# Kernel tuning notes

Measured on AMD Instinct MI355X. Metric: run time of the kernel, lower is better.

The kernel has to match this reference:

```python
import jax, jax.numpy as jnp
import numpy as np
import math

B, T, D_IN, D_F, H = 256, 64, 2048, 2048, 512


def _uniform(key, shape, stdv):
    return jax.random.uniform(key, shape, jnp.float32, -stdv, stdv)


def setup_inputs() -> dict:
    key = jax.random.key(0)
    ks = jax.random.split(key, 16)
    stdv = 1.0 / math.sqrt(H)
    return {
        "input_feats": jax.random.normal(ks[0], (B, T, D_IN), jnp.float32),
        "aux0": jax.random.normal(ks[1], (B, T, D_F), jnp.float32),
        "W_ih": _uniform(ks[2], (3 * H, D_IN), stdv),
        "b_ih": _uniform(ks[3], (3 * H,), stdv),
        "W_fh0": _uniform(ks[4], (2 * H, D_F), stdv),
        "b_fh0": _uniform(ks[5], (2 * H,), stdv),
        "W_hh": _uniform(ks[6], (3 * H, H), stdv),
        "b_hh": _uniform(ks[7], (3 * H,), stdv),
        "Wq": _uniform(ks[8], (H, H), stdv),
        "bq": _uniform(ks[9], (H,), stdv),
        "Wk": _uniform(ks[10], (H, H), stdv),
        "bk": _uniform(ks[11], (H,), stdv),
        "Wv": _uniform(ks[12], (H, H), stdv),
        "bv": _uniform(ks[13], (H,), stdv),
    }


def _gru_gcc_forward(input_feats, aux0, W_ih, b_ih, W_fh0, b_fh0, W_hh, b_hh,
                     Wq, bq, Wk, bk, Wv, bv):
    # Precompute input and aux projections for all timesteps (big batched GEMMs).
    gi_all = jnp.einsum('btd,gd->btg', input_feats, W_ih) + b_ih   # [B,T,3H]
    gf_all = jnp.einsum('btd,gd->btg', aux0, W_fh0) + b_fh0        # [B,T,2H]
    scale = 1.0 / math.sqrt(H)

    def attend(q, kv_in):
        # q: [B,1,H], kv_in: [B,S,H] raw gate candidates (keys == values)
        k = jnp.einsum('bsh,oh->bso', kv_in, Wk) + bk
        v = jnp.einsum('bsh,oh->bso', kv_in, Wv) + bv
        scores = jnp.einsum('bqh,bsh->bqs', q, k) * scale
        p = jax.nn.softmax(scores, axis=-1)
        return jnp.einsum('bqs,bsh->bqh', p, v)[:, 0, :]  # [B,H]

    def step(hx, xs):
        gi_t, gf_t = xs  # [B,3H], [B,2H]
        gh = hx @ W_hh.T + b_hh
        i_r, i_i, i_n = jnp.split(gi_t, 3, axis=1)
        h_r, h_i, h_n = jnp.split(gh, 3, axis=1)
        t1, t2 = jnp.split(gf_t, 2, axis=1)
        q = jnp.einsum('bqh,oh->bqo', hx[:, None, :], Wq) + bq  # [B,1,H]
        keys_r = jnp.stack([t1, i_r], axis=1)  # [B,2,H]
        keys_i = jnp.stack([t2, i_i], axis=1)
        resetgate = jax.nn.sigmoid(attend(q, keys_r) + h_r)
        inputgate = jax.nn.sigmoid(attend(q, keys_i) + h_i)
        newgate = jnp.tanh(i_n + resetgate * h_n)
        hy = newgate + inputgate * (hx - newgate)
        return hy, hy

    hx0 = jnp.zeros((input_feats.shape[0], H), input_feats.dtype)
    xs = (jnp.swapaxes(gi_all, 0, 1), jnp.swapaxes(gf_all, 0, 1))  # time-major
    h_last, out = jax.lax.scan(step, hx0, xs)
    return jnp.swapaxes(out, 0, 1), h_last  # [B,T,H], [B,H]


def reference(input_feats, aux0, W_ih, b_ih, W_fh0, b_fh0, W_hh, b_hh,
              Wq, bq, Wk, bk, Wv, bv):
    return _gru_gcc_forward(input_feats, aux0, W_ih, b_ih, W_fh0, b_fh0,
                            W_hh, b_hh, Wq, bq, Wk, bk, Wv, bv)
```

## Files before the change

kernel.cpp:

```cpp
#include <hip/hip_runtime.h>
#include <hip/hip_bf16.h>
#include <cstdint>
#include <cstddef>

#define B_    256
#define T_    64
#define H_    512
#define DIN_  2048
#define BT_   (B_ * T_)
#define NPRE_ 2560
#define NCAT_ 2048
#define NV_   2048

typedef __attribute__((ext_vector_type(8))) __bf16 bf16x8;
typedef __attribute__((ext_vector_type(4))) float  f32x4;

__device__ __forceinline__ float bf2f(unsigned short u) {
    union { unsigned int i; float f; } v; v.i = ((unsigned int)u) << 16; return v.f;
}
__device__ __forceinline__ unsigned short f2bf(float f) {
    union { float f; unsigned int i; } v; v.f = f;
    unsigned int x = v.i;
    return (unsigned short)((x + 0x7fffu + ((x >> 16) & 1u)) >> 16);
}

__device__ __forceinline__ void gload_lds16(const unsigned short* g, unsigned short* l) {
    __builtin_amdgcn_global_load_lds(
        (const __attribute__((address_space(1))) void*)g,
        (__attribute__((address_space(3))) void*)l, 16, 0, 0);
}

__global__ void cast4_kernel(const float* __restrict__ src,
                             unsigned short* __restrict__ dst, int n4) {
    int i = blockIdx.x * blockDim.x + threadIdx.x;
    if (i >= n4) return;
    const float4 v = ((const float4*)src)[i];
    ushort4 o;
    o.x = f2bf(v.x); o.y = f2bf(v.y); o.z = f2bf(v.z); o.w = f2bf(v.w);
    ((ushort4*)dst)[i] = o;
}

__global__ __launch_bounds__(256)
void wqk_kernel(const float* __restrict__ Wk, const float* __restrict__ Wq,
                unsigned short* __restrict__ Wout) {
    __shared__ float sk[16][17], sq[16][17];
    const int tid = threadIdx.x;
    const int tx = tid & 15, ty = tid >> 4;
    const int j0 = blockIdx.y * 16, h0 = blockIdx.x * 16;
    float acc = 0.f;
    for (int o0 = 0; o0 < 512; o0 += 16) {
        sk[ty][tx] = Wk[(o0 + ty) * 512 + j0 + tx];
        sq[ty][tx] = Wq[(o0 + ty) * 512 + h0 + tx];
        __syncthreads();
        #pragma unroll
        for (int oo = 0; oo < 16; oo++)
            acc = fmaf(sk[oo][ty], sq[oo][tx], acc);
        __syncthreads();
    }
    Wout[(size_t)(j0 + ty) * 512 + h0 + tx] = f2bf(acc);
}

__global__ void bqk_kernel(const float* __restrict__ Wk, const float* __restrict__ bq,
                           float* __restrict__ bout) {
    int j = blockIdx.x * 64 + threadIdx.x;
    float acc = 0.f;
    for (int o = 0; o < 512; o++)
        acc = fmaf(Wk[o * 512 + j], bq[o], acc);
    bout[j] = acc;
}

__global__ __launch_bounds__(256)
void gemm_rec(const unsigned short* __restrict__ A,
              const unsigned short* __restrict__ W,
              const float* __restrict__ bias,
              float* __restrict__ C, int N, int K) {
    const int n0 = blockIdx.x * 128;
    const int m0 = blockIdx.y * 64;
    const int tid = threadIdx.x;
    const int wave = tid >> 6, lane = tid & 63;
    const int wm = (wave >> 1) * 32, wn = (wave & 1) * 64;
    const int row16 = lane & 15;
    const int kq = (lane >> 4) * 8;

    f32x4 acc[2][4];
    #pragma unroll
    for (int i = 0; i < 2; i++)
        #pragma unroll
        for (int j = 0; j < 4; j++) {
            acc[i][j].x = 0.f; acc[i][j].y = 0.f; acc[i][j].z = 0.f; acc[i][j].w = 0.f;
        }

    const unsigned short* a_base = A + (size_t)(m0 + wm + row16) * K + kq;
    const unsigned short* b_base = W + (size_t)(n0 + wn + row16) * K + kq;

    #pragma unroll 2
    for (int k = 0; k < K; k += 32) {
        bf16x8 a[2], b[4];
        #pragma unroll
        for (int i = 0; i < 2; i++)
            a[i] = *(const bf16x8*)(const void*)(a_base + (size_t)i * 16 * K + k);
        #pragma unroll
        for (int j = 0; j < 4; j++)
            b[j] = *(const bf16x8*)(const void*)(b_base + (size_t)j * 16 * K + k);
        #pragma unroll
        for (int i = 0; i < 2; i++)
            #pragma unroll
            for (int j = 0; j < 4; j++)
                acc[i][j] = __builtin_amdgcn_mfma_f32_16x16x32_bf16(a[i], b[j], acc[i][j], 0, 0, 0);
    }

    const int col = lane & 15;
    const int rbase = (lane >> 4) * 4;
    #pragma unroll
    for (int i = 0; i < 2; i++) {
        #pragma unroll
        for (int j = 0; j < 4; j++) {
            const int n = n0 + wn + j * 16 + col;
            const float bb = bias[n];
            #pragma unroll
            for (int r = 0; r < 4; r++) {
                const int m = m0 + wm + i * 16 + rbase + r;
                C[(size_t)m * N + n] = acc[i][j][r] + bb;
            }
        }
    }
}

__global__ __launch_bounds__(256)
void gemm_lds(const unsigned short* __restrict__ A0,
              const unsigned short* __restrict__ A1, int nsplit,
              const unsigned short* __restrict__ W,
              const float* __restrict__ bias,
              float* __restrict__ C,
              unsigned short* __restrict__ Apk, int N, int K) {
    __shared__ unsigned short sA[128 * 32];
    __shared__ unsigned short sB[128 * 32];
    const int n0 = blockIdx.x * 128;
    const int m0 = blockIdx.y * 128;
    const unsigned short* A = (n0 < nsplit) ? A0 : A1;
    const int tid = threadIdx.x;
    const int wave = tid >> 6, lane = tid & 63;
    const int wm = (wave >> 1) * 64, wn = (wave & 1) * 64;
    const int row16 = lane & 15;
    const int kq = (lane >> 4) * 8;

    f32x4 acc[4][4];
    #pragma unroll
    for (int i = 0; i < 4; i++)
        #pragma unroll
        for (int j = 0; j < 4; j++) {
            acc[i][j].x = 0.f; acc[i][j].y = 0.f; acc[i][j].z = 0.f; acc[i][j].w = 0.f;
        }

    const int srow = tid >> 2;
    const int scol = (tid & 3) * 8;
    const unsigned short* gA0 = A + (size_t)(m0 + srow) * K + scol;
    const unsigned short* gA1 = A + (size_t)(m0 + 64 + srow) * K + scol;
    const unsigned short* gB0 = W + (size_t)(n0 + srow) * K + scol;
    const unsigned short* gB1 = W + (size_t)(n0 + 64 + srow) * K + scol;
    unsigned short* dA0 = sA + tid * 8;
    unsigned short* dA1 = sA + 2048 + tid * 8;
    unsigned short* dB0 = sB + tid * 8;
    unsigned short* dB1 = sB + 2048 + tid * 8;

    for (int k = 0; k < K; k += 32) {
        gload_lds16(gA0 + k, dA0);
        gload_lds16(gA1 + k, dA1);
        gload_lds16(gB0 + k, dB0);
        gload_lds16(gB1 + k, dB1);
        __syncthreads();
        bf16x8 a[4], b[4];
        #pragma unroll
        for (int i = 0; i < 4; i++)
            a[i] = *(const bf16x8*)(const void*)(sA + (wm + i * 16 + row16) * 32 + kq);
        #pragma unroll
        for (int j = 0; j < 4; j++)
            b[j] = *(const bf16x8*)(const void*)(sB + (wn + j * 16 + row16) * 32 + kq);
        #pragma unroll
        for (int i = 0; i < 4; i++)
            #pragma unroll
            for (int j = 0; j < 4; j++)
                acc[i][j] = __builtin_amdgcn_mfma_f32_16x16x32_bf16(a[i], b[j], acc[i][j], 0, 0, 0);
        __syncthreads();
    }

    int pbase = -1;
    if (n0 >= 1536 && n0 < 2048)      pbase = n0 - 1536;
    else if (n0 < 512)                pbase = n0 + 512;
    else if (n0 >= 2048)              pbase = n0 - 1024;
    else if (n0 >= 512 && n0 < 1024)  pbase = n0 + 1024;

    const int col = lane & 15;
    const int rbase = (lane >> 4) * 4;
    #pragma unroll
    for (int i = 0; i < 4; i++) {
        #pragma unroll
        for (int j = 0; j < 4; j++) {
            const int nloc = wn + j * 16 + col;
            const int n = n0 + nloc;
            const float bb = bias[n];
            #pragma unroll
            for (int r = 0; r < 4; r++) {
                const int m = m0 + wm + i * 16 + rbase + r;
                const float val = acc[i][j][r] + bb;
                C[(size_t)m * N + n] = val;
                if (pbase >= 0)
                    Apk[(size_t)m * NV_ + pbase + nloc] = f2bf(val);
            }
        }
    }
}

__global__ __launch_bounds__(256)
void gemm_v(const unsigned short* __restrict__ Apk,
            const unsigned short* __restrict__ Wvbf,
            const float* __restrict__ bv,
            unsigned short* __restrict__ Vbf) {
    __shared__ unsigned short sA[128 * 32];
    __shared__ unsigned short sB[128 * 32];
    const int n0 = blockIdx.x * 128;
    const int m0 = blockIdx.y * 128;
    const int aoff = n0 & ~511;
    const int nb0 = n0 & 511;
    const int tid = threadIdx.x;
    const int wave = tid >> 6, lane = tid & 63;
    const int wm = (wave >> 1) * 64, wn = (wave & 1) * 64;
    const int row16 = lane & 15;
    const int kq = (lane >> 4) * 8;

    f32x4 acc[4][4];
    #pragma unroll
    for (int i = 0; i < 4; i++)
        #pragma unroll
        for (int j = 0; j < 4; j++) {
            acc[i][j].x = 0.f; acc[i][j].y = 0.f; acc[i][j].z = 0.f; acc[i][j].w = 0.f;
        }

    const int srow = tid >> 2;
    const int scol = (tid & 3) * 8;
    const unsigned short* gA0 = Apk + (size_t)(m0 + srow) * NV_ + aoff + scol;
    const unsigned short* gA1 = Apk + (size_t)(m0 + 64 + srow) * NV_ + aoff + scol;
    const unsigned short* gB0 = Wvbf + (size_t)(nb0 + srow) * 512 + scol;
    const unsigned short* gB1 = Wvbf + (size_t)(nb0 + 64 + srow) * 512 + scol;
    unsigned short* dA0 = sA + tid * 8;
    unsigned short* dA1 = sA + 2048 + tid * 8;
    unsigned short* dB0 = sB + tid * 8;
    unsigned short* dB1 = sB + 2048 + tid * 8;

    for (int k = 0; k < 512; k += 32) {
        gload_lds16(gA0 + k, dA0);
        gload_lds16(gA1 + k, dA1);
        gload_lds16(gB0 + k, dB0);
        gload_lds16(gB1 + k, dB1);
        __syncthreads();
        bf16x8 a[4], b[4];
        #pragma unroll
        for (int i = 0; i < 4; i++)
            a[i] = *(const bf16x8*)(const void*)(sA + (wm + i * 16 + row16) * 32 + kq);
        #pragma unroll
        for (int j = 0; j < 4; j++)
            b[j] = *(const bf16x8*)(const void*)(sB + (wn + j * 16 + row16) * 32 + kq);
        #pragma unroll
        for (int i = 0; i < 4; i++)
            #pragma unroll
            for (int j = 0; j < 4; j++)
                acc[i][j] = __builtin_amdgcn_mfma_f32_16x16x32_bf16(a[i], b[j], acc[i][j], 0, 0, 0);
        __syncthreads();
    }

    const int col = lane & 15;
    const int rbase = (lane >> 4) * 4;
    #pragma unroll
    for (int i = 0; i < 4; i++) {
        #pragma unroll
        for (int j = 0; j < 4; j++) {
            const int nloc = wn + j * 16 + col;
            const float bb = bv[nb0 + nloc];
            #pragma unroll
            for (int r = 0; r < 4; r++) {
                const int m = m0 + wm + i * 16 + rbase + r;
                Vbf[(size_t)m * NV_ + n0 + nloc] = f2bf(acc[i][j][r] + bb);
            }
        }
    }
}

__global__ __launch_bounds__(512)
void attn_gates2(const float* __restrict__ comb,
                 const float* __restrict__ Cpre,
                 const unsigned short* __restrict__ Vbf,
                 float* __restrict__ hx,
                 unsigned short* __restrict__ hxbf,
                 float* __restrict__ out,
                 int t) {
    __shared__ float red0[8], red1[8], red2[8], red3[8];
    const int b = blockIdx.x;
    const int h = threadIdx.x;
    const int lane = h & 63, wv = h >> 6;
    const float* combRow = comb + (size_t)b * NCAT_;
    const float* pre = Cpre + (size_t)(b * T_ + t) * NPRE_;
    const unsigned short* vrow = Vbf + (size_t)(b * T_ + t) * NV_;

    const float q  = combRow[1536 + h];
    const float t1 = pre[1536 + h];
    const float ir = pre[h];
    const float t2 = pre[2048 + h];
    const float ii = pre[512 + h];

    float pr0 = q * t1, pr1 = q * ir, pi0 = q * t2, pi1 = q * ii;
    #pragma unroll
    for (int off = 32; off > 0; off >>= 1) {
        pr0 += __shfl_down(pr0, off);
        pr1 += __shfl_down(pr1, off);
        pi0 += __shfl_down(pi0, off);
        pi1 += __shfl_down(pi1, off);
    }
    if (lane == 0) { red0[wv] = pr0; red1[wv] = pr1; red2[wv] = pi0; red3[wv] = pi1; }
    __syncthreads();
    float s_r0 = 0.f, s_r1 = 0.f, s_i0 = 0.f, s_i1 = 0.f;
    #pragma unroll
    for (int w = 0; w < 8; w++) {
        s_r0 += red0[w]; s_r1 += red1[w]; s_i0 += red2[w]; s_i1 += red3[w];
    }
    const float scale = 0.04419417382415922f;
    const float prob_r0 = 1.f / (1.f + expf((s_r1 - s_r0) * scale));
    const float prob_i0 = 1.f / (1.f + expf((s_i1 - s_i0) * scale));

    const float vt1 = bf2f(vrow[h]);
    const float vir = bf2f(vrow[512 + h]);
    const float vt2 = bf2f(vrow[1024 + h]);
    const float vii = bf2f(vrow[1536 + h]);
    const float cr = prob_r0 * vt1 + (1.f - prob_r0) * vir;
    const float ci = prob_i0 * vt2 + (1.f - prob_i0) * vii;

    const float rg = 1.f / (1.f + expf(-(cr + combRow[h])));
    const float ig = 1.f / (1.f + expf(-(ci + combRow[512 + h])));
    const float i_n = pre[1024 + h];
    const float hn  = combRow[1024 + h];
    const float ng  = tanhf(fmaf(rg, hn, i_n));
    const float hxv = hx[(size_t)b * H_ + h];
    const float hy  = ng + ig * (hxv - ng);
    out[(size_t)(b * T_ + t) * H_ + h] = hy;
    hx[(size_t)b * H_ + h] = hy;
    hxbf[(size_t)b * H_ + h] = f2bf(hy);
    if (t == T_ - 1)
        out[(size_t)B_ * T_ * H_ + (size_t)b * H_ + h] = hy;
}

extern "C" void kernel_launch(void* const* d_in, const int* in_sizes, int n_in,
                              void* d_out, int out_size, void* d_ws, size_t ws_size,
                              hipStream_t stream) {
    const float* input_feats = (const float*)d_in[0];
    const float* aux0   = (const float*)d_in[1];
    const float* W_ih   = (const float*)d_in[2];
    const float* b_ih   = (const float*)d_in[3];
    const float* W_fh0  = (const float*)d_in[4];
    const float* b_fh0  = (const float*)d_in[5];
    const float* W_hh   = (const float*)d_in[6];
    const float* b_hh   = (const float*)d_in[7];
    const float* Wq     = (const float*)d_in[8];
    const float* bq     = (const float*)d_in[9];
    const float* Wk     = (const float*)d_in[10];
    const float* Wv     = (const float*)d_in[12];
    const float* bv     = (const float*)d_in[13];
    float* out = (float*)d_out;

    char* ws = (char*)d_ws;
    size_t off = 0;
    auto alloc = [&](size_t bytes) -> void* {
        void* p = ws + off;
        off += (bytes + 255) & ~(size_t)255;
        return p;
    };
    unsigned short* Xbf  = (unsigned short*)alloc((size_t)BT_ * DIN_ * 2);
    unsigned short* Vbf  = Xbf;
    unsigned short* Abf  = (unsigned short*)alloc((size_t)BT_ * DIN_ * 2);
    unsigned short* Wpre = (unsigned short*)alloc((size_t)NPRE_ * DIN_ * 2);
    float*          Cpre = (float*)alloc((size_t)BT_ * NPRE_ * 4);
    unsigned short* Apk  = (unsigned short*)alloc((size_t)BT_ * NV_ * 2);
    unsigned short* Wcat = (unsigned short*)alloc((size_t)NCAT_ * H_ * 2);
    unsigned short* Wvbf = (unsigned short*)alloc((size_t)H_ * H_ * 2);
    float* bpre = (float*)alloc((size_t)NPRE_ * 4);
    float* bcat = (float*)alloc((size_t)NCAT_ * 4);
    float* comb = (float*)alloc((size_t)B_ * NCAT_ * 4);
    float* hx   = (float*)alloc((size_t)B_ * H_ * 4);
    unsigned short* hxbf = (unsigned short*)alloc((size_t)B_ * H_ * 2);

    hipMemsetAsync(hx, 0, (size_t)B_ * H_ * 4, stream);
    hipMemsetAsync(hxbf, 0, (size_t)B_ * H_ * 2, stream);

    auto cast = [&](const float* s, unsigned short* d, size_t n) {
        int n4 = (int)(n / 4);
        cast4_kernel<<<(n4 + 255) / 256, 256, 0, stream>>>(s, d, n4);
    };
    cast(input_feats, Xbf, (size_t)BT_ * DIN_);
    cast(aux0, Abf, (size_t)BT_ * DIN_);
    cast(W_ih, Wpre, (size_t)1536 * DIN_);
    cast(W_fh0, Wpre + (size_t)1536 * DIN_, (size_t)1024 * DIN_);
    cast(W_hh, Wcat, (size_t)1536 * H_);
    cast(Wv, Wvbf, (size_t)H_ * H_);

    hipMemcpyAsync(bpre, b_ih, 1536 * 4, hipMemcpyDeviceToDevice, stream);
    hipMemcpyAsync(bpre + 1536, b_fh0, 1024 * 4, hipMemcpyDeviceToDevice, stream);
    hipMemcpyAsync(bcat, b_hh, 1536 * 4, hipMemcpyDeviceToDevice, stream);

    wqk_kernel<<<dim3(32, 32), 256, 0, stream>>>(Wk, Wq, Wcat + (size_t)1536 * H_);
    bqk_kernel<<<8, 64, 0, stream>>>(Wk, bq, bcat + 1536);

    gemm_lds<<<dim3(NPRE_ / 128, BT_ / 128), 256, 0, stream>>>(
        Xbf, Abf, 1536, Wpre, bpre, Cpre, Apk, NPRE_, DIN_);

    gemm_v<<<dim3(NV_ / 128, BT_ / 128), 256, 0, stream>>>(Apk, Wvbf, bv, Vbf);

    for (int t = 0; t < T_; t++) {
        gemm_rec<<<dim3(NCAT_ / 128, B_ / 64), 256, 0, stream>>>(
            hxbf, Wcat, bcat, comb, NCAT_, H_);
        attn_gates2<<<B_, H_, 0, stream>>>(comb, Cpre, Vbf, hx, hxbf, out, t);
    }
}
```

Measured before the change: 1.902 ms.

## Fuse recurrent GEMM and gate steps into one persistent cooperative kernel

Replaces the 128 per-timestep launches (recurrent GEMM plus attention/gate kernel) with a single cooperative persistent kernel of 256 blocks. Each block computes a 32x64 tile of the hidden projection, grid-syncs, then updates one batch row's gates and hidden state, with the hidden state kept in registers instead of a global fp32 buffer. This removes per-step launch overhead, but every step now pays two grid-wide barriers and the GEMM runs with fewer waves per tile.

```diff
diff --git a/kernel.cpp b/kernel.cpp
--- a/kernel.cpp
+++ b/kernel.cpp
@@ -1,7 +1,10 @@
 #include <hip/hip_runtime.h>
 #include <hip/hip_bf16.h>
+#include <hip/hip_cooperative_groups.h>
 #include <cstdint>
 #include <cstddef>
+
+namespace cg = cooperative_groups;
 
 #define B_    256
 #define T_    64
@@ -67,63 +70,6 @@
     for (int o = 0; o < 512; o++)
         acc = fmaf(Wk[o * 512 + j], bq[o], acc);
     bout[j] = acc;
-}
-
-__global__ __launch_bounds__(256)
-void gemm_rec(const unsigned short* __restrict__ A,
-              const unsigned short* __restrict__ W,
-              const float* __restrict__ bias,
-              float* __restrict__ C, int N, int K) {
-    const int n0 = blockIdx.x * 128;
-    const int m0 = blockIdx.y * 64;
-    const int tid = threadIdx.x;
-    const int wave = tid >> 6, lane = tid & 63;
-    const int wm = (wave >> 1) * 32, wn = (wave & 1) * 64;
-    const int row16 = lane & 15;
-    const int kq = (lane >> 4) * 8;
-
-    f32x4 acc[2][4];
-    #pragma unroll
-    for (int i = 0; i < 2; i++)
-        #pragma unroll
-        for (int j = 0; j < 4; j++) {
-            acc[i][j].x = 0.f; acc[i][j].y = 0.f; acc[i][j].z = 0.f; acc[i][j].w = 0.f;
-        }
-
-    const unsigned short* a_base = A + (size_t)(m0 + wm + row16) * K + kq;
-    const unsigned short* b_base = W + (size_t)(n0 + wn + row16) * K + kq;
-
-    #pragma unroll 2
-    for (int k = 0; k < K; k += 32) {
-        bf16x8 a[2], b[4];
-        #pragma unroll
-        for (int i = 0; i < 2; i++)
-            a[i] = *(const bf16x8*)(const void*)(a_base + (size_t)i * 16 * K + k);
-        #pragma unroll
-        for (int j = 0; j < 4; j++)
-            b[j] = *(const bf16x8*)(const void*)(b_base + (size_t)j * 16 * K + k);
-        #pragma unroll
-        for (int i = 0; i < 2; i++)
-            #pragma unroll
-            for (int j = 0; j < 4; j++)
-                acc[i][j] = __builtin_amdgcn_mfma_f32_16x16x32_bf16(a[i], b[j], acc[i][j], 0, 0, 0);
-    }
-
-    const int col = lane & 15;
-    const int rbase = (lane >> 4) * 4;
-    #pragma unroll
-    for (int i = 0; i < 2; i++) {
-        #pragma unroll
-        for (int j = 0; j < 4; j++) {
-            const int n = n0 + wn + j * 16 + col;
-            const float bb = bias[n];
-            #pragma unroll
-            for (int r = 0; r < 4; r++) {
-                const int m = m0 + wm + i * 16 + rbase + r;
-                C[(size_t)m * N + n] = acc[i][j][r] + bb;
-            }
-        }
-    }
 }
 
 __global__ __launch_bounds__(256)
@@ -285,66 +231,111 @@
     }
 }
 
-__global__ __launch_bounds__(512)
-void attn_gates2(const float* __restrict__ comb,
+__global__ __launch_bounds__(256)
+void loop_kernel(unsigned short* __restrict__ hxbf,
+                 const unsigned short* __restrict__ Wcat,
+                 const float* __restrict__ bcat,
+                 float* __restrict__ comb,
                  const float* __restrict__ Cpre,
                  const unsigned short* __restrict__ Vbf,
-                 float* __restrict__ hx,
-                 unsigned short* __restrict__ hxbf,
-                 float* __restrict__ out,
-                 int t) {
-    __shared__ float red0[8], red1[8], red2[8], red3[8];
-    const int b = blockIdx.x;
-    const int h = threadIdx.x;
-    const int lane = h & 63, wv = h >> 6;
-    const float* combRow = comb + (size_t)b * NCAT_;
-    const float* pre = Cpre + (size_t)(b * T_ + t) * NPRE_;
-    const unsigned short* vrow = Vbf + (size_t)(b * T_ + t) * NV_;
-
-    const float q  = combRow[1536 + h];
-    const float t1 = pre[1536 + h];
-    const float ir = pre[h];
-    const float t2 = pre[2048 + h];
-    const float ii = pre[512 + h];
-
-    float pr0 = q * t1, pr1 = q * ir, pi0 = q * t2, pi1 = q * ii;
-    #pragma unroll
-    for (int off = 32; off > 0; off >>= 1) {
-        pr0 += __shfl_down(pr0, off);
-        pr1 += __shfl_down(pr1, off);
-        pi0 += __shfl_down(pi0, off);
-        pi1 += __shfl_down(pi1, off);
-    }
-    if (lane == 0) { red0[wv] = pr0; red1[wv] = pr1; red2[wv] = pi0; red3[wv] = pi1; }
-    __syncthreads();
-    float s_r0 = 0.f, s_r1 = 0.f, s_i0 = 0.f, s_i1 = 0.f;
-    #pragma unroll
-    for (int w = 0; w < 8; w++) {
-        s_r0 += red0[w]; s_r1 += red1[w]; s_i0 += red2[w]; s_i1 += red3[w];
-    }
+                 float* __restrict__ out) {
+    cg::grid_group grid = cg::this_grid();
+    const int bid = blockIdx.x;
+    const int tid = threadIdx.x;
+    const int wave = tid >> 6, lane = tid & 63;
+
+    const int m0 = (bid >> 5) * 32, n0 = (bid & 31) * 64;
+    const int wr = wave & 1, wc = wave >> 1;
+    const int row16 = lane & 15, kq = (lane >> 4) * 8;
+    const int col = lane & 15, rbase = (lane >> 4) * 4;
+    const unsigned short* abase = hxbf + (size_t)(m0 + wr * 16 + row16) * H_ + kq;
+    const unsigned short* bbase = Wcat + (size_t)(n0 + wc * 32 + row16) * H_ + kq;
+    const int nc0 = n0 + wc * 32 + col;
+    const float bb0 = bcat[nc0], bb1 = bcat[nc0 + 16];
+
+    const int b = bid;
+    const int h0 = tid, h1 = tid + 256;
+    float hy0 = 0.f, hy1 = 0.f;
+    __shared__ float red[4][4];
     const float scale = 0.04419417382415922f;
-    const float prob_r0 = 1.f / (1.f + expf((s_r1 - s_r0) * scale));
-    const float prob_i0 = 1.f / (1.f + expf((s_i1 - s_i0) * scale));
-
-    const float vt1 = bf2f(vrow[h]);
-    const float vir = bf2f(vrow[512 + h]);
-    const float vt2 = bf2f(vrow[1024 + h]);
-    const float vii = bf2f(vrow[1536 + h]);
-    const float cr = prob_r0 * vt1 + (1.f - prob_r0) * vir;
-    const float ci = prob_i0 * vt2 + (1.f - prob_i0) * vii;
-
-    const float rg = 1.f / (1.f + expf(-(cr + combRow[h])));
-    const float ig = 1.f / (1.f + expf(-(ci + combRow[512 + h])));
-    const float i_n = pre[1024 + h];
-    const float hn  = combRow[1024 + h];
-    const float ng  = tanhf(fmaf(rg, hn, i_n));
-    const float hxv = hx[(size_t)b * H_ + h];
-    const float hy  = ng + ig * (hxv - ng);
-    out[(size_t)(b * T_ + t) * H_ + h] = hy;
-    hx[(size_t)b * H_ + h] = hy;
-    hxbf[(size_t)b * H_ + h] = f2bf(hy);
-    if (t == T_ - 1)
-        out[(size_t)B_ * T_ * H_ + (size_t)b * H_ + h] = hy;
+
+    for (int t = 0; t < T_; t++) {
+        f32x4 acc0 = {0.f, 0.f, 0.f, 0.f}, acc1 = {0.f, 0.f, 0.f, 0.f};
+        #pragma unroll 4
+        for (int k = 0; k < H_; k += 32) {
+            bf16x8 av  = *(const bf16x8*)(const void*)(abase + k);
+            bf16x8 b0v = *(const bf16x8*)(const void*)(bbase + k);
+            bf16x8 b1v = *(const bf16x8*)(const void*)(bbase + (size_t)16 * H_ + k);
+            acc0 = __builtin_amdgcn_mfma_f32_16x16x32_bf16(av, b0v, acc0, 0, 0, 0);
+            acc1 = __builtin_amdgcn_mfma_f32_16x16x32_bf16(av, b1v, acc1, 0, 0, 0);
+        }
+        #pragma unroll
+        for (int r = 0; r < 4; r++) {
+            const int m = m0 + wr * 16 + rbase + r;
+            comb[(size_t)m * NCAT_ + nc0]      = acc0[r] + bb0;
+            comb[(size_t)m * NCAT_ + nc0 + 16] = acc1[r] + bb1;
+        }
+        grid.sync();
+
+        const float* combRow = comb + (size_t)b * NCAT_;
+        const float* pre = Cpre + (size_t)(b * T_ + t) * NPRE_;
+        const unsigned short* vrow = Vbf + (size_t)(b * T_ + t) * NV_;
+
+        const float q0  = combRow[1536 + h0], q1  = combRow[1536 + h1];
+        const float t1a = pre[1536 + h0],     t1b = pre[1536 + h1];
+        const float ira = pre[h0],            irb = pre[h1];
+        const float t2a = pre[2048 + h0],     t2b = pre[2048 + h1];
+        const float iia = pre[512 + h0],      iib = pre[512 + h1];
+
+        float pr0 = q0 * t1a + q1 * t1b;
+        float pr1 = q0 * ira + q1 * irb;
+        float pi0 = q0 * t2a + q1 * t2b;
+        float pi1 = q0 * iia + q1 * iib;
+        #pragma unroll
+        for (int off = 32; off > 0; off >>= 1) {
+            pr0 += __shfl_down(pr0, off);
+            pr1 += __shfl_down(pr1, off);
+            pi0 += __shfl_down(pi0, off);
+            pi1 += __shfl_down(pi1, off);
+        }
+        if (lane == 0) {
+            red[wave][0] = pr0; red[wave][1] = pr1;
+            red[wave][2] = pi0; red[wave][3] = pi1;
+        }
+        __syncthreads();
+        const float s_r0 = red[0][0] + red[1][0] + red[2][0] + red[3][0];
+        const float s_r1 = red[0][1] + red[1][1] + red[2][1] + red[3][1];
+        const float s_i0 = red[0][2] + red[1][2] + red[2][2] + red[3][2];
+        const float s_i1 = red[0][3] + red[1][3] + red[2][3] + red[3][3];
+        const float prob_r0 = 1.f / (1.f + expf((s_r1 - s_r0) * scale));
+        const float prob_i0 = 1.f / (1.f + expf((s_i1 - s_i0) * scale));
+
+        {
+            const float cr = prob_r0 * bf2f(vrow[h0]) + (1.f - prob_r0) * bf2f(vrow[512 + h0]);
+            const float ci = prob_i0 * bf2f(vrow[1024 + h0]) + (1.f - prob_i0) * bf2f(vrow[1536 + h0]);
+            const float rg = 1.f / (1.f + expf(-(cr + combRow[h0])));
+            const float ig = 1.f / (1.f + expf(-(ci + combRow[512 + h0])));
+            const float ng = tanhf(fmaf(rg, combRow[1024 + h0], pre[1024 + h0]));
+            hy0 = ng + ig * (hy0 - ng);
+            out[(size_t)(b * T_ + t) * H_ + h0] = hy0;
+            hxbf[(size_t)b * H_ + h0] = f2bf(hy0);
+        }
+        {
+            const float cr = prob_r0 * bf2f(vrow[h1]) + (1.f - prob_r0) * bf2f(vrow[512 + h1]);
+            const float ci = prob_i0 * bf2f(vrow[1024 + h1]) + (1.f - prob_i0) * bf2f(vrow[1536 + h1]);
+            const float rg = 1.f / (1.f + expf(-(cr + combRow[h1])));
+            const float ig = 1.f / (1.f + expf(-(ci + combRow[512 + h1])));
+            const float ng = tanhf(fmaf(rg, combRow[1024 + h1], pre[1024 + h1]));
+            hy1 = ng + ig * (hy1 - ng);
+            out[(size_t)(b * T_ + t) * H_ + h1] = hy1;
+            hxbf[(size_t)b * H_ + h1] = f2bf(hy1);
+        }
+        if (t == T_ - 1) {
+            out[(size_t)B_ * T_ * H_ + (size_t)b * H_ + h0] = hy0;
+            out[(size_t)B_ * T_ * H_ + (size_t)b * H_ + h1] = hy1;
+        }
+        grid.sync();
+    }
 }
 
 extern "C" void kernel_launch(void* const* d_in, const int* in_sizes, int n_in,
@@ -363,7 +354,7 @@
     const float* Wk     = (const float*)d_in[10];
     const float* Wv     = (const float*)d_in[12];
     const float* bv     = (const float*)d_in[13];
-    float* out = (float*)d_out;
+    float* outp = (float*)d_out;
 
     char* ws = (char*)d_ws;
     size_t off = 0;
@@ -383,10 +374,8 @@
     float* bpre = (float*)alloc((size_t)NPRE_ * 4);
     float* bcat = (float*)alloc((size_t)NCAT_ * 4);
     float* comb = (float*)alloc((size_t)B_ * NCAT_ * 4);
-    float* hx   = (float*)alloc((size_t)B_ * H_ * 4);
     unsigned short* hxbf = (unsigned short*)alloc((size_t)B_ * H_ * 2);
 
-    hipMemsetAsync(hx, 0, (size_t)B_ * H_ * 4, stream);
     hipMemsetAsync(hxbf, 0, (size_t)B_ * H_ * 2, stream);
 
     auto cast = [&](const float* s, unsigned short* d, size_t n) {
@@ -412,9 +401,10 @@
 
     gemm_v<<<dim3(NV_ / 128, BT_ / 128), 256, 0, stream>>>(Apk, Wvbf, bv, Vbf);
 
-    for (int t = 0; t < T_; t++) {
-        gemm_rec<<<dim3(NCAT_ / 128, B_ / 64), 256, 0, stream>>>(
-            hxbf, Wcat, bcat, comb, NCAT_, H_);
-        attn_gates2<<<B_, H_, 0, stream>>>(comb, Cpre, Vbf, hx, hxbf, out, t);
-    }
-}
+    {
+        void* cargs[] = {(void*)&hxbf, (void*)&Wcat, (void*)&bcat, (void*)&comb,
+                         (void*)&Cpre, (void*)&Vbf, (void*)&outp};
+        hipLaunchCooperativeKernel((const void*)loop_kernel, dim3(256), dim3(256),
+                                   cargs, 0, stream);
+    }
+}
```

Result: slower. 5.226 ms (+174.8%).
